# Kernel tuning notes

Hardware: AMD Instinct MI355X
Metric: run time of the kernel (lower is better)

Reference implementation:

```python
import jax, jax.numpy as jnp
import numpy as np

B, C, IMG, P = 64, 3, 224, 16
D, L, H, DH, M, NC = 768, 12, 12, 64, 3072, 1000
INNER = H * DH
PD = C * P * P          # patch_dim = 768
NP = (IMG // P) ** 2    # 196 patches


def setup_inputs() -> dict:
    key = jax.random.key(0)
    ks = jax.random.split(key, 16)
    s = 0.02
    nrm = lambda k, shape: jax.random.normal(k, shape, jnp.float32) * s
    return dict(
        img=jax.random.normal(ks[0], (B, C, IMG, IMG), jnp.float32),
        patch_ln1_g=jnp.ones(PD), patch_ln1_b=jnp.zeros(PD),
        patch_w=nrm(ks[1], (PD, D)), patch_b=jnp.zeros(D),
        patch_ln2_g=jnp.ones(D), patch_ln2_b=jnp.zeros(D),
        pos_emb=nrm(ks[2], (1, NP + 1, D)),
        cls_tok=nrm(ks[3], (1, 1, D)),
        attn_ln_g=jnp.ones((L, D)), attn_ln_b=jnp.zeros((L, D)),
        w_qkv=nrm(ks[4], (L, D, 3 * INNER)),
        w_out=nrm(ks[5], (L, INNER, D)), b_out=jnp.zeros((L, D)),
        ff_ln_g=jnp.ones((L, D)), ff_ln_b=jnp.zeros((L, D)),
        ff_w1=nrm(ks[6], (L, D, M)), ff_b1=jnp.zeros((L, M)),
        ff_w2=nrm(ks[7], (L, M, D)), ff_b2=jnp.zeros((L, D)),
        final_ln_g=jnp.ones(D), final_ln_b=jnp.zeros(D),
        head_w=nrm(ks[8], (D, NC)), head_b=jnp.zeros(NC),
    )


def _ln(x, g, b, eps=1e-5):
    m = x.mean(-1, keepdims=True)
    v = ((x - m) ** 2).mean(-1, keepdims=True)
    return (x - m) / jnp.sqrt(v + eps) * g + b


def reference(img, patch_ln1_g, patch_ln1_b, patch_w, patch_b, patch_ln2_g,
              patch_ln2_b, pos_emb, cls_tok, attn_ln_g, attn_ln_b, w_qkv,
              w_out, b_out, ff_ln_g, ff_ln_b, ff_w1, ff_b1, ff_w2, ff_b2,
              final_ln_g, final_ln_b, head_w, head_b):
    b, c, hh, ww = img.shape
    h, w = hh // P, ww // P
    # Rearrange 'b c (h p1) (w p2) -> b (h w) (p1 p2 c)'
    x = img.reshape(b, c, h, P, w, P).transpose(0, 2, 4, 3, 5, 1).reshape(b, h * w, P * P * c)
    x = _ln(x, patch_ln1_g, patch_ln1_b)
    x = x @ patch_w + patch_b
    x = _ln(x, patch_ln2_g, patch_ln2_b)
    n = x.shape[1]
    x = jnp.concatenate([jnp.broadcast_to(cls_tok, (b, 1, x.shape[-1])), x], axis=1)
    x = x + pos_emb[:, : n + 1]
    scale = DH ** -0.5
    for l in range(L):
        xn = _ln(x, attn_ln_g[l], attn_ln_b[l])
        qkv = xn @ w_qkv[l]  # [b, n+1, 3*inner]
        q, k, v = jnp.split(qkv, 3, axis=-1)
        sp = lambda t: t.reshape(b, -1, H, DH).transpose(0, 2, 1, 3)  # b h n d
        q, k, v = sp(q), sp(k), sp(v)
        # softmax variant: exp(scores*scale), normalize by sum + eps (no max-subtract, faithful to source)
        numer = jnp.exp(jnp.einsum('bhid,bhjd->bhij', q, k) * scale)
        attn = numer / (numer.sum(-1, keepdims=True) + 1e-8)
        out = jnp.einsum('bhij,bhjd->bhid', attn, v)
        out = out.transpose(0, 2, 1, 3).reshape(b, -1, INNER)
        x = out @ w_out[l] + b_out[l] + x
        xn = _ln(x, ff_ln_g[l], ff_ln_b[l])
        hid = jax.nn.gelu(xn @ ff_w1[l] + ff_b1[l], approximate=False)
        x = hid @ ff_w2[l] + ff_b2[l] + x
    x = _ln(x, final_ln_g, final_ln_b)
    return x[:, 0] @ head_w + head_b
```

## Files before the change

### kernel.cpp

```cpp
#include <hip/hip_runtime.h>
#include <hip/hip_bf16.h>
#include <math.h>

#define B_     64
#define NTOK   197
#define NPATCH 196
#define D768   768
#define NL     12
#define NH     12
#define MFF    3072
#define NCLS   1000
#define ROWS   (B_ * NTOK)
#define PROWS  (B_ * NPATCH)
#define ROWS_PAD 12672

typedef unsigned short ushort;
typedef __bf16 bf16x8 __attribute__((ext_vector_type(8)));
typedef float  f32x4  __attribute__((ext_vector_type(4)));
typedef unsigned short u16x4 __attribute__((ext_vector_type(4)));
typedef unsigned short u16x2 __attribute__((ext_vector_type(2)));

__device__ __forceinline__ ushort f2b(float f) {
  __hip_bfloat16 h = __float2bfloat16(f);
  return *reinterpret_cast<ushort*>(&h);
}
__device__ __forceinline__ float b2f(ushort u) {
  unsigned int v = ((unsigned int)u) << 16;
  float f;
  __builtin_memcpy(&f, &v, 4);
  return f;
}

__device__ __forceinline__ void gload16(const ushort* g, ushort* lds) {
  __builtin_amdgcn_global_load_lds((const __attribute__((address_space(1))) void*)g,
                                   (__attribute__((address_space(3))) void*)lds, 16, 0, 0);
}

__device__ __forceinline__ float gelu_f(float v) {
  float t = v * fmaf(0.0713548162726f, v * v, 1.5957691216f);
  return v / (1.0f + __expf(-t));
}

__device__ __forceinline__ void block_mean_rstd(float s, float sq, float& mean, float& rstd) {
#pragma unroll
  for (int off = 32; off; off >>= 1) { s += __shfl_xor(s, off); sq += __shfl_xor(sq, off); }
  __shared__ float ss[4], ssq[4];
  int w = threadIdx.x >> 6;
  if ((threadIdx.x & 63) == 0) { ss[w] = s; ssq[w] = sq; }
  __syncthreads();
  s  = ss[0] + ss[1] + ss[2] + ss[3];
  sq = ssq[0] + ssq[1] + ssq[2] + ssq[3];
  mean = s * (1.0f / 768.0f);
  float var = sq * (1.0f / 768.0f) - mean * mean;
  rstd = rsqrtf(var + 1e-5f);
}

__global__ __launch_bounds__(256) void ln_rows_b(const ushort* __restrict__ in, long in_stride,
                                                 const float* __restrict__ g,
                                                 const float* __restrict__ bta,
                                                 ushort* __restrict__ out) {
  const ushort* xr = in + (size_t)blockIdx.x * in_stride;
  int t = threadIdx.x;
  float v0 = 0.f, v1 = 0.f, v2 = 0.f, v3 = 0.f;
  if (t < 192) {
    u16x4 xv = *(const u16x4*)(xr + t * 4);
    v0 = b2f(xv[0]); v1 = b2f(xv[1]); v2 = b2f(xv[2]); v3 = b2f(xv[3]);
  }
  float mean, rstd;
  block_mean_rstd(v0 + v1 + v2 + v3,
                  v0 * v0 + v1 * v1 + v2 * v2 + v3 * v3, mean, rstd);
  if (t < 192) {
    f32x4 gv = *(const f32x4*)(g + t * 4);
    f32x4 bv = *(const f32x4*)(bta + t * 4);
    u16x4 o = { f2b((v0 - mean) * rstd * gv[0] + bv[0]),
                f2b((v1 - mean) * rstd * gv[1] + bv[1]),
                f2b((v2 - mean) * rstd * gv[2] + bv[2]),
                f2b((v3 - mean) * rstd * gv[3] + bv[3]) };
    *(u16x4*)(out + (size_t)blockIdx.x * 768 + t * 4) = o;
  }
}

__global__ __launch_bounds__(256) void patch_ln1(const float* __restrict__ img,
                                                 const float* __restrict__ g,
                                                 const float* __restrict__ bta,
                                                 ushort* __restrict__ xp) {
  int pidx = blockIdx.x;
  int b = pidx / NPATCH, hw = pidx % NPATCH;
  int ph = hw / 14, pw = hw % 14;
  int t = threadIdx.x;
  float v[3];
#pragma unroll
  for (int u = 0; u < 3; ++u) {
    int k = t + u * 256;
    int c = k % 3, p2 = (k / 3) & 15, p1 = k / 48;
    v[u] = img[(((size_t)b * 3 + c) * 224 + ph * 16 + p1) * 224 + pw * 16 + p2];
  }
  float mean, rstd;
  block_mean_rstd(v[0] + v[1] + v[2], v[0] * v[0] + v[1] * v[1] + v[2] * v[2], mean, rstd);
  ushort* o = xp + (size_t)pidx * 768;
#pragma unroll
  for (int u = 0; u < 3; ++u) { int k = t + u * 256; o[k] = f2b((v[u] - mean) * rstd * g[k] + bta[k]); }
}

__global__ __launch_bounds__(256) void ln2_pos(const float* __restrict__ xe,
                                               const float* __restrict__ g,
                                               const float* __restrict__ bta,
                                               const float* __restrict__ pos,
                                               ushort* __restrict__ x) {
  int pidx = blockIdx.x;
  int b = pidx / NPATCH, i = pidx % NPATCH;
  const float* xr = xe + (size_t)pidx * 768;
  int t = threadIdx.x;
  float v0 = xr[t], v1 = xr[t + 256], v2 = xr[t + 512];
  float mean, rstd;
  block_mean_rstd(v0 + v1 + v2, v0 * v0 + v1 * v1 + v2 * v2, mean, rstd);
  const float* p = pos + (size_t)(1 + i) * 768;
  ushort* o = x + ((size_t)b * NTOK + 1 + i) * 768;
  o[t]       = f2b((v0 - mean) * rstd * g[t]       + bta[t]       + p[t]);
  o[t + 256] = f2b((v1 - mean) * rstd * g[t + 256] + bta[t + 256] + p[t + 256]);
  o[t + 512] = f2b((v2 - mean) * rstd * g[t + 512] + bta[t + 512] + p[t + 512]);
}

__global__ __launch_bounds__(256) void cls_init(const float* __restrict__ cls_tok,
                                                const float* __restrict__ pos,
                                                ushort* __restrict__ x) {
  int b = blockIdx.x, t = threadIdx.x;
  ushort* o = x + (size_t)b * NTOK * 768;
#pragma unroll
  for (int u = 0; u < 3; ++u) { int k = t + u * 256; o[k] = f2b(cls_tok[k] + pos[k]); }
}

__global__ __launch_bounds__(256) void transpose_cast(const float* __restrict__ W,
                                                      ushort* __restrict__ Wt,
                                                      int K, int N) {
  __shared__ float t[32][33];
  int n0 = blockIdx.x * 32, k0 = blockIdx.y * 32;
  int tx = threadIdx.x, ty = threadIdx.y;
#pragma unroll
  for (int u = 0; u < 32; u += 8) {
    int n = n0 + tx;
    t[ty + u][tx] = (n < N) ? W[(size_t)(k0 + ty + u) * N + n] : 0.f;
  }
  __syncthreads();
#pragma unroll
  for (int u = 0; u < 32; u += 8) {
    int n = n0 + ty + u;
    if (n < N) Wt[(size_t)n * K + k0 + tx] = f2b(t[tx][ty + u]);
  }
}

__device__ __forceinline__ void transpose_layer64(int bid,
                                                  const float* wq, const float* wo,
                                                  const float* w1, const float* w2,
                                                  ushort* tq, ushort* to,
                                                  ushort* t1, ushort* t2) {
  const float* W; ushort* Wt; int K, N, xt;
  if (bid < 432)       {             W = wq; Wt = tq; K = 768;  N = 2304; xt = 36; }
  else if (bid < 576)  { bid -= 432; W = wo; Wt = to; K = 768;  N = 768;  xt = 12; }
  else if (bid < 1152) { bid -= 576; W = w1; Wt = t1; K = 768;  N = 3072; xt = 48; }
  else                 { bid -= 1152; W = w2; Wt = t2; K = 3072; N = 768; xt = 12; }
  int n0 = (bid % xt) * 64, k0 = (bid / xt) * 64;
  __shared__ float t[64][65];
  int id = threadIdx.x;
  int tx = id & 15, ty = id >> 4;
#pragma unroll
  for (int u = 0; u < 4; ++u) {
    int k = ty + 16 * u;
    f32x4 v = *(const f32x4*)(W + (size_t)(k0 + k) * N + n0 + tx * 4);
    t[k][tx * 4 + 0] = v[0]; t[k][tx * 4 + 1] = v[1];
    t[k][tx * 4 + 2] = v[2]; t[k][tx * 4 + 3] = v[3];
  }
  __syncthreads();
  int wx = id & 31, wy = id >> 5;
#pragma unroll
  for (int u = 0; u < 8; ++u) {
    int n = wy + 8 * u;
    u16x2 o = { f2b(t[wx * 2][n]), f2b(t[wx * 2 + 1][n]) };
    *(u16x2*)(Wt + (size_t)(n0 + n) * K + k0 + wx * 2) = o;
  }
}

__global__ __launch_bounds__(256) void transpose4(const float* __restrict__ wq,
                                                  const float* __restrict__ wo,
                                                  const float* __restrict__ w1,
                                                  const float* __restrict__ w2,
                                                  ushort* __restrict__ tq,
                                                  ushort* __restrict__ to,
                                                  ushort* __restrict__ t1,
                                                  ushort* __restrict__ t2) {
  transpose_layer64(blockIdx.x, wq, wo, w1, w2, tq, to, t1, t2);
}

__global__ __launch_bounds__(256) void transpose_all(const float* __restrict__ wq,
                                                     const float* __restrict__ wo,
                                                     const float* __restrict__ w1,
                                                     const float* __restrict__ w2,
                                                     ushort* __restrict__ tq,
                                                     ushort* __restrict__ to,
                                                     ushort* __restrict__ t1,
                                                     ushort* __restrict__ t2) {
  int l = blockIdx.x / 1728, bid = blockIdx.x % 1728;
  transpose_layer64(bid,
                    wq + (size_t)l * 768 * 2304, wo + (size_t)l * 768 * 768,
                    w1 + (size_t)l * 768 * MFF,  w2 + (size_t)l * MFF * 768,
                    tq + (size_t)l * 2304 * 768, to + (size_t)l * 768 * 768,
                    t1 + (size_t)l * MFF * 768,  t2 + (size_t)l * 768 * MFF);
}

template<int EP, int RESID, int OBF>
__global__ __launch_bounds__(256, 4) void gemm_v6(const ushort* __restrict__ A,
                                                  const ushort* __restrict__ Bt,
                                                  const float* __restrict__ bias,
                                                  const void* __restrict__ resid,
                                                  void* __restrict__ Cv,
                                                  int M, int N, int K) {
  __shared__ ushort smem[2 * 8192];

  const int tid = threadIdx.x;
  const int w = tid >> 6, l = tid & 63;
  const int fr = l & 15, fc = l >> 4;

  const int ntx = gridDim.x;
  const int nwg = ntx * gridDim.y;
  const int orig = blockIdx.y * ntx + blockIdx.x;
  const int q = nwg >> 3, r = nwg & 7, xcd = orig & 7, idx = orig >> 3;
  const int wg = (xcd < r ? xcd * (q + 1) : r * (q + 1) + (xcd - r) * q) + idx;
  const int row0 = (wg / ntx) * 128, col0 = (wg % ntx) * 128;

  const int wr = (w >> 1) * 64, wc = (w & 1) * 64;

  const int srow = tid >> 2;
  const int sg = (tid & 3) ^ ((srow >> 1) & 3);
  const ushort* pA0 = A  + (size_t)(row0 + srow) * K + sg * 8;
  const ushort* pA1 = A  + (size_t)(row0 + 64 + srow) * K + sg * 8;
  const ushort* pB0 = Bt + (size_t)(col0 + srow) * K + sg * 8;
  const ushort* pB1 = Bt + (size_t)(col0 + 64 + srow) * K + sg * 8;

  auto stage = [&](int t_, ushort* dst) {
    const int k0 = t_ * 32;
    gload16(pA0 + k0, dst + tid * 8);
    gload16(pA1 + k0, dst + (tid + 256) * 8);
    gload16(pB0 + k0, dst + 4096 + tid * 8);
    gload16(pB1 + k0, dst + 4096 + (tid + 256) * 8);
  };

  int idxA[4], idxB[4];
#pragma unroll
  for (int m = 0; m < 4; ++m) {
    int rA = wr + m * 16 + fr;
    idxA[m] = rA * 32 + ((fc ^ ((rA >> 1) & 3)) << 3);
  }
#pragma unroll
  for (int n = 0; n < 4; ++n) {
    int rB = wc + n * 16 + fr;
    idxB[n] = rB * 32 + ((fc ^ ((rB >> 1) & 3)) << 3);
  }

  f32x4 acc[4][4] = {};

  auto compute = [&](const ushort* As) {
    const ushort* Bs = As + 4096;
    bf16x8 a_[4], b_[4];
#pragma unroll
    for (int m = 0; m < 4; ++m) a_[m] = *(const bf16x8*)(As + idxA[m]);
#pragma unroll
    for (int n = 0; n < 4; ++n) b_[n] = *(const bf16x8*)(Bs + idxB[n]);
#pragma unroll
    for (int m = 0; m < 4; ++m)
#pragma unroll
      for (int n = 0; n < 4; ++n)
        acc[m][n] = __builtin_amdgcn_mfma_f32_16x16x32_bf16(b_[n], a_[m], acc[m][n], 0, 0, 0);
  };

#define VM4() asm volatile("s_waitcnt vmcnt(4)" ::: "memory")
#define VM0() asm volatile("s_waitcnt vmcnt(0)" ::: "memory")

  const int NT = K >> 5;

  stage(0, smem);
  for (int t = 0; t < NT; t += 2) {
    if (t + 1 < NT) { stage(t + 1, smem + 8192); VM4(); } else VM0();
    __builtin_amdgcn_s_barrier();
    compute(smem);
    __builtin_amdgcn_s_barrier();
    if (t + 1 < NT) {
      if (t + 2 < NT) { stage(t + 2, smem); VM4(); } else VM0();
      __builtin_amdgcn_s_barrier();
      compute(smem + 8192);
      __builtin_amdgcn_s_barrier();
    }
  }
#undef VM4
#undef VM0

  if (!OBF) {
    float* Cf = (float*)Cv;
#pragma unroll
    for (int m = 0; m < 4; ++m) {
      int row = row0 + wr + m * 16 + fr;
      if (row >= M) continue;
#pragma unroll
      for (int n = 0; n < 4; ++n) {
        int col = col0 + wc + n * 16 + fc * 4;
        f32x4 v = acc[m][n];
        if (bias) v += *(const f32x4*)(bias + col);
        if (EP) {
#pragma unroll
          for (int rr = 0; rr < 4; ++rr) v[rr] = gelu_f(v[rr]);
        }
        if (RESID) v += *(const f32x4*)((const float*)resid + (size_t)row * N + col);
        *(f32x4*)(Cf + (size_t)row * N + col) = v;
      }
    }
  } else {
    __syncthreads();
    ushort* Cw = smem + w * 4096;
#pragma unroll
    for (int m = 0; m < 4; ++m) {
      int rl = m * 16 + fr;
      int row = row0 + wr + rl;
#pragma unroll
      for (int n = 0; n < 4; ++n) {
        int col = col0 + wc + n * 16 + fc * 4;
        f32x4 v = acc[m][n];
        if (bias) v += *(const f32x4*)(bias + col);
        if (EP) {
#pragma unroll
          for (int rr = 0; rr < 4; ++rr) v[rr] = gelu_f(v[rr]);
        }
        if (RESID) {
          u16x4 rv = *(const u16x4*)((const ushort*)resid + (size_t)row * N + col);
#pragma unroll
          for (int rr = 0; rr < 4; ++rr) v[rr] += b2f(rv[rr]);
        }
        u16x4 pk = { f2b(v[0]), f2b(v[1]), f2b(v[2]), f2b(v[3]) };
        int s = (n * 4 + fc) ^ (rl & 7);
        *(u16x4*)(Cw + rl * 64 + s * 4) = pk;
      }
    }
    ushort* Cb = (ushort*)Cv;
#pragma unroll
    for (int pp = 0; pp < 16; ++pp) {
      int rl = pp * 4 + (l >> 4);
      int cs = l & 15;
      u16x4 pk = *(const u16x4*)(Cw + rl * 64 + ((cs ^ (rl & 7)) * 4));
      int row = row0 + wr + rl;
      if (row < M) *(u16x4*)(Cb + (size_t)row * N + col0 + wc + cs * 4) = pk;
    }
  }
}

template<int EP, int RESID, int OBF>
__global__ __launch_bounds__(256, 2) void gemm_v7(const ushort* __restrict__ A,
                                                  const ushort* __restrict__ Bt,
                                                  const float* __restrict__ bias,
                                                  const float* __restrict__ resid,
                                                  void* __restrict__ Cv,
                                                  int M, int N, int K) {
  __shared__ ushort smem[2 * 12288];

  const int tid = threadIdx.x;
  const int w = tid >> 6, l = tid & 63;
  const int fr = l & 15, fc = l >> 4;

  const int ntx = gridDim.x;
  const int nwg = ntx * gridDim.y;
  const int orig = blockIdx.y * ntx + blockIdx.x;
  const int q = nwg >> 3, r = nwg & 7, xcd = orig & 7, idx = orig >> 3;
  const int wg = (xcd < r ? xcd * (q + 1) : r * (q + 1) + (xcd - r) * q) + idx;
  const int row0 = (wg / ntx) * 128, col0 = (wg % ntx) * 256;

  const int wrow = (w >> 1) * 64, wcol = (w & 1) * 128;

  const int srow = tid >> 2;
  const int sg = (tid & 3) ^ ((srow >> 1) & 3);
  const ushort* pA0 = A  + (size_t)(row0 + srow) * K + sg * 8;
  const ushort* pA1 = A  + (size_t)(row0 + 64 + srow) * K + sg * 8;
  const ushort* pB0 = Bt + (size_t)(col0 + srow) * K + sg * 8;
  const ushort* pB1 = Bt + (size_t)(col0 + 64 + srow) * K + sg * 8;
  const ushort* pB2 = Bt + (size_t)(col0 + 128 + srow) * K + sg * 8;
  const ushort* pB3 = Bt + (size_t)(col0 + 192 + srow) * K + sg * 8;

  auto stage = [&](int t_, ushort* dst) {
    const int k0 = t_ * 32;
    gload16(pA0 + k0, dst + tid * 8);
    gload16(pA1 + k0, dst + (tid + 256) * 8);
    ushort* db = dst + 4096;
    gload16(pB0 + k0, db + tid * 8);
    gload16(pB1 + k0, db + (tid + 256) * 8);
    gload16(pB2 + k0, db + (tid + 512) * 8);
    gload16(pB3 + k0, db + (tid + 768) * 8);
  };

  int idxA[4], idxB[8];
#pragma unroll
  for (int m = 0; m < 4; ++m) {
    int rA = wrow + m * 16 + fr;
    idxA[m] = rA * 32 + ((fc ^ ((rA >> 1) & 3)) << 3);
  }
#pragma unroll
  for (int n = 0; n < 8; ++n) {
    int rB = wcol + n * 16 + fr;
    idxB[n] = rB * 32 + ((fc ^ ((rB >> 1) & 3)) << 3);
  }

  f32x4 acc[4][8] = {};

  auto compute = [&](const ushort* As) {
    const ushort* Bs = As + 4096;
    bf16x8 a_[4], b_[8];
#pragma unroll
    for (int m = 0; m < 4; ++m) a_[m] = *(const bf16x8*)(As + idxA[m]);
#pragma unroll
    for (int n = 0; n < 8; ++n) b_[n] = *(const bf16x8*)(Bs + idxB[n]);
#pragma unroll
    for (int m = 0; m < 4; ++m)
#pragma unroll
      for (int n = 0; n < 8; ++n)
        acc[m][n] = __builtin_amdgcn_mfma_f32_16x16x32_bf16(b_[n], a_[m], acc[m][n], 0, 0, 0);
  };

#define VM6() asm volatile("s_waitcnt vmcnt(6)" ::: "memory")
#define VM0() asm volatile("s_waitcnt vmcnt(0)" ::: "memory")

  const int NT = K >> 5;

  stage(0, smem);
  for (int t = 0; t < NT; t += 2) {
    if (t + 1 < NT) { stage(t + 1, smem + 12288); VM6(); } else VM0();
    __builtin_amdgcn_s_barrier();
    compute(smem);
    __builtin_amdgcn_s_barrier();
    if (t + 1 < NT) {
      if (t + 2 < NT) { stage(t + 2, smem); VM6(); } else VM0();
      __builtin_amdgcn_s_barrier();
      compute(smem + 12288);
      __builtin_amdgcn_s_barrier();
    }
  }
#undef VM6
#undef VM0

  if (!OBF) {
    float* Cf = (float*)Cv;
#pragma unroll
    for (int m = 0; m < 4; ++m) {
      int row = row0 + wrow + m * 16 + fr;
      if (row >= M) continue;
#pragma unroll
      for (int n = 0; n < 8; ++n) {
        int col = col0 + wcol + n * 16 + fc * 4;
        f32x4 v = acc[m][n];
        if (bias) v += *(const f32x4*)(bias + col);
        if (EP) {
#pragma unroll
          for (int rr = 0; rr < 4; ++rr) v[rr] = gelu_f(v[rr]);
        }
        if (RESID) v += *(const f32x4*)(resid + (size_t)row * N + col);
        *(f32x4*)(Cf + (size_t)row * N + col) = v;
      }
    }
  } else {
    ushort* Cw = smem + w * 4096;
    ushort* Cb = (ushort*)Cv;
#pragma unroll
    for (int mp = 0; mp < 2; ++mp) {
#pragma unroll
      for (int m2 = 0; m2 < 2; ++m2) {
        int m = mp * 2 + m2;
        int rl = m2 * 16 + fr;
#pragma unroll
        for (int n = 0; n < 8; ++n) {
          int col = col0 + wcol + n * 16 + fc * 4;
          f32x4 v = acc[m][n];
          if (bias) v += *(const f32x4*)(bias + col);
          if (EP) {
#pragma unroll
            for (int rr = 0; rr < 4; ++rr) v[rr] = gelu_f(v[rr]);
          }
          u16x4 pk = { f2b(v[0]), f2b(v[1]), f2b(v[2]), f2b(v[3]) };
          int s = (n * 4 + fc) ^ (rl & 7);
          *(u16x4*)(Cw + rl * 128 + s * 4) = pk;
        }
      }
      asm volatile("s_waitcnt lgkmcnt(0)" ::: "memory");
#pragma unroll
      for (int pp = 0; pp < 16; ++pp) {
        int rl = pp * 2 + (l >> 5);
        int cs = l & 31;
        u16x4 pk = *(const u16x4*)(Cw + rl * 128 + ((cs ^ (rl & 7)) * 4));
        int row = row0 + wrow + mp * 32 + rl;
        if (row < M) *(u16x4*)(Cb + (size_t)row * N + col0 + wcol + cs * 4) = pk;
      }
      asm volatile("s_waitcnt lgkmcnt(0)" ::: "memory");
    }
  }
}

template<int EP, int RESID, int OBF>
__global__ __launch_bounds__(256) void gemm_bt(const ushort* __restrict__ A,
                                               const ushort* __restrict__ Bt,
                                               const float* __restrict__ bias,
                                               const float* __restrict__ resid,
                                               void* __restrict__ C,
                                               int M, int N, int K) {
  __shared__ ushort As[128 * 32];
  __shared__ ushort Bs[128 * 32];
  int tid = threadIdx.x;
  int w = tid >> 6, l = tid & 63;
  int fr = l & 15, fc = l >> 4;
  int row0 = blockIdx.y * 128, col0 = blockIdx.x * 128;
  int wr = (w >> 1) * 64, wc = (w & 1) * 64;

  int srow0 = w * 32 + (l >> 2);
  int srow1 = srow0 + 16;
  int sc0 = (((l & 3) ^ ((srow0 >> 1) & 3)) << 3);
  int sc1 = (((l & 3) ^ ((srow1 >> 1) & 3)) << 3);
  const ushort* ga0 = A  + (size_t)(row0 + srow0) * K + sc0;
  const ushort* ga1 = A  + (size_t)(row0 + srow1) * K + sc1;
  const ushort* gb0 = Bt + (size_t)(col0 + srow0) * K + sc0;
  const ushort* gb1 = Bt + (size_t)(col0 + srow1) * K + sc1;

  int idxA[4], idxB[4];
#pragma unroll
  for (int m = 0; m < 4; ++m) {
    int rA = wr + m * 16 + fr;
    idxA[m] = rA * 32 + ((fc ^ ((rA >> 1) & 3)) << 3);
  }
#pragma unroll
  for (int n = 0; n < 4; ++n) {
    int rB = wc + n * 16 + fr;
    idxB[n] = rB * 32 + ((fc ^ ((rB >> 1) & 3)) << 3);
  }

  f32x4 acc[4][4] = {};

  for (int k0 = 0; k0 < K; k0 += 32) {
    gload16(ga0 + k0, &As[w * 1024]);
    gload16(ga1 + k0, &As[w * 1024 + 512]);
    gload16(gb0 + k0, &Bs[w * 1024]);
    gload16(gb1 + k0, &Bs[w * 1024 + 512]);
    __syncthreads();
    bf16x8 af[4], bfr[4];
#pragma unroll
    for (int m = 0; m < 4; ++m) af[m] = *(const bf16x8*)(As + idxA[m]);
#pragma unroll
    for (int n = 0; n < 4; ++n) bfr[n] = *(const bf16x8*)(Bs + idxB[n]);
#pragma unroll
    for (int m = 0; m < 4; ++m)
#pragma unroll
      for (int n = 0; n < 4; ++n)
        acc[m][n] = __builtin_amdgcn_mfma_f32_16x16x32_bf16(af[m], bfr[n], acc[m][n], 0, 0, 0);
    __syncthreads();
  }

#pragma unroll
  for (int n = 0; n < 4; ++n) {
    int col = col0 + wc + n * 16 + fr;
    if (col >= N) continue;
    float bv = bias ? bias[col] : 0.f;
#pragma unroll
    for (int m = 0; m < 4; ++m) {
#pragma unroll
      for (int rr = 0; rr < 4; ++rr) {
        int row = row0 + wr + m * 16 + fc * 4 + rr;
        if (row >= M) continue;
        float v = acc[m][n][rr] + bv;
        if (EP == 1) v = 0.5f * v * (1.0f + erff(v * 0.70710678118654752f));
        if (RESID) v += resid[(size_t)row * N + col];
        if (OBF) ((ushort*)C)[(size_t)row * N + col] = f2b(v);
        else     ((float*)C)[(size_t)row * N + col]  = v;
      }
    }
  }
}

__global__ __launch_bounds__(256) void attn_mfma(const ushort* __restrict__ qkv,
                                                 ushort* __restrict__ aout) {
  int bid = blockIdx.x;
  int qt = bid & 3;
  int h  = (bid >> 2) % NH;
  int b  = (bid >> 2) / NH;
  int tid = threadIdx.x, w = tid >> 6, l = tid & 63;
  int fr = l & 15, fc = l >> 4;

  __shared__ ushort Vt[64 * 64];
  __shared__ ushort Pl[4 * 16 * 64];

  const size_t brow = (size_t)b * NTOK;
  int q0 = qt * 64 + w * 16;

  bf16x8 qf[2];
  {
    const ushort* qp = qkv + (brow + q0 + fr) * 2304 + h * 64 + fc * 8;
    qf[0] = *(const bf16x8*)qp;
    qf[1] = *(const bf16x8*)(qp + 32);
  }
  float rs[4] = {0.f, 0.f, 0.f, 0.f};
  f32x4 oc[4] = {};

  for (int kt = 0; kt < 4; ++kt) {
    __syncthreads();
    {
      int key = tid >> 2, d0 = (tid & 3) * 16;
      int j = kt * 64 + key;
      bool valid = j < NTOK;
      const ushort* vp = qkv + (brow + j) * 2304 + 1536 + h * 64 + d0;
      ushort vbuf[16];
      if (valid) {
        *(bf16x8*)(vbuf)     = *(const bf16x8*)vp;
        *(bf16x8*)(vbuf + 8) = *(const bf16x8*)(vp + 8);
      } else {
#pragma unroll
        for (int i = 0; i < 16; ++i) vbuf[i] = 0;
      }
#pragma unroll
      for (int i = 0; i < 16; ++i) {
        int d = d0 + i;
        int byte = d * 128 + ((((key >> 3)) ^ (d & 7)) << 4) + (key & 7) * 2;
        Vt[byte >> 1] = vbuf[i];
      }
    }
    f32x4 sc[4];
#pragma unroll
    for (int n = 0; n < 4; ++n) {
      f32x4 z = {};
      const ushort* kp = qkv + (brow + kt * 64 + n * 16 + fr) * 2304 + 768 + h * 64 + fc * 8;
      bf16x8 k0 = *(const bf16x8*)kp;
      bf16x8 k1 = *(const bf16x8*)(kp + 32);
      z = __builtin_amdgcn_mfma_f32_16x16x32_bf16(qf[0], k0, z, 0, 0, 0);
      z = __builtin_amdgcn_mfma_f32_16x16x32_bf16(qf[1], k1, z, 0, 0, 0);
      sc[n] = z;
    }
    float part[4] = {0.f, 0.f, 0.f, 0.f};
#pragma unroll
    for (int n = 0; n < 4; ++n) {
      int j = kt * 64 + n * 16 + fr;
      bool jv = j < NTOK;
#pragma unroll
      for (int rr = 0; rr < 4; ++rr) {
        float e = jv ? __expf(sc[n][rr] * 0.125f) : 0.f;
        part[rr] += e;
        int row = fc * 4 + rr, col = n * 16 + fr;
        int byte = row * 128 + (((col >> 3) ^ (row & 7)) << 4) + (col & 7) * 2;
        Pl[w * 1024 + (byte >> 1)] = f2b(e);
      }
    }
#pragma unroll
    for (int rr = 0; rr < 4; ++rr) {
      float p = part[rr];
      p += __shfl_xor(p, 1); p += __shfl_xor(p, 2);
      p += __shfl_xor(p, 4); p += __shfl_xor(p, 8);
      rs[rr] += p;
    }
    __syncthreads();
#pragma unroll
    for (int ks = 0; ks < 2; ++ks) {
      int prow = fr;
      int pbyte = prow * 128 + (((ks * 4 + fc) ^ (prow & 7)) << 4);
      bf16x8 pf = *(const bf16x8*)(Pl + w * 1024 + (pbyte >> 1));
#pragma unroll
      for (int n = 0; n < 4; ++n) {
        int d = n * 16 + fr;
        int vb = d * 128 + (((ks * 4 + fc) ^ (d & 7)) << 4);
        bf16x8 vf = *(const bf16x8*)(Vt + (vb >> 1));
        oc[n] = __builtin_amdgcn_mfma_f32_16x16x32_bf16(pf, vf, oc[n], 0, 0, 0);
      }
    }
  }
#pragma unroll
  for (int n = 0; n < 4; ++n) {
#pragma unroll
    for (int rr = 0; rr < 4; ++rr) {
      int qq = q0 + fc * 4 + rr;
      if (qq < NTOK) {
        float v = oc[n][rr] / (rs[rr] + 1e-8f);
        aout[(brow + qq) * 768 + h * 64 + n * 16 + fr] = f2b(v);
      }
    }
  }
}

extern "C" void kernel_launch(void* const* d_in, const int* in_sizes, int n_in,
                              void* d_out, int out_size, void* d_ws, size_t ws_size,
                              hipStream_t stream) {
  const float* img       = (const float*)d_in[0];
  const float* p_ln1_g   = (const float*)d_in[1];
  const float* p_ln1_b   = (const float*)d_in[2];
  const float* patch_w   = (const float*)d_in[3];
  const float* patch_b   = (const float*)d_in[4];
  const float* p_ln2_g   = (const float*)d_in[5];
  const float* p_ln2_b   = (const float*)d_in[6];
  const float* pos_emb   = (const float*)d_in[7];
  const float* cls_tok   = (const float*)d_in[8];
  const float* attn_ln_g = (const float*)d_in[9];
  const float* attn_ln_b = (const float*)d_in[10];
  const float* w_qkv     = (const float*)d_in[11];
  const float* w_out     = (const float*)d_in[12];
  const float* b_out     = (const float*)d_in[13];
  const float* ff_ln_g   = (const float*)d_in[14];
  const float* ff_ln_b   = (const float*)d_in[15];
  const float* ff_w1     = (const float*)d_in[16];
  const float* ff_b1     = (const float*)d_in[17];
  const float* ff_w2     = (const float*)d_in[18];
  const float* ff_b2     = (const float*)d_in[19];
  const float* fin_ln_g  = (const float*)d_in[20];
  const float* fin_ln_b  = (const float*)d_in[21];
  const float* head_w    = (const float*)d_in[22];
  const float* head_b    = (const float*)d_in[23];
  float* out = (float*)d_out;

  char* p = (char*)d_ws;
  auto alloc = [&](size_t bytes) { char* r = p; p += (bytes + 255) & ~(size_t)255; return r; };
  ushort* x      = (ushort*)alloc((size_t)ROWS_PAD * 768 * 2);
  ushort* xnb    = (ushort*)alloc((size_t)ROWS_PAD * 768 * 2);
  ushort* qkvb   = (ushort*)alloc((size_t)ROWS_PAD * 2304 * 2);
  ushort* aoutb  = (ushort*)alloc((size_t)ROWS_PAD * 768 * 2);
  ushort* pwt    = (ushort*)alloc((size_t)768 * 768 * 2);
  ushort* hwt    = (ushort*)alloc((size_t)1024 * 768 * 2);
  ushort* xclsb  = (ushort*)alloc((size_t)128 * 768 * 2);
  ushort* hidb   = qkvb;
  ushort* xpb    = xnb;
  float*  xe     = (float*)qkvb;

  const size_t SQ = (size_t)2304 * 768, SO = (size_t)768 * 768, S1 = (size_t)MFF * 768;
  size_t used = (size_t)(p - (char*)d_ws);
  bool oneshot = (used + 12 * (SQ + SO + 2 * S1) * 2 + 4096) <= ws_size;
  int nw = oneshot ? 12 : 1;
  ushort* wtq = (ushort*)alloc(nw * SQ * 2);
  ushort* wto = (ushort*)alloc(nw * SO * 2);
  ushort* wt1 = (ushort*)alloc(nw * S1 * 2);
  ushort* wt2 = (ushort*)alloc(nw * S1 * 2);

  dim3 blk(256), tblk(32, 8);

  transpose_cast<<<dim3(24, 24), tblk, 0, stream>>>(patch_w, pwt, 768, 768);
  transpose_cast<<<dim3(32, 24), tblk, 0, stream>>>(head_w, hwt, 768, 1000);
  if (oneshot)
    transpose_all<<<12 * 1728, blk, 0, stream>>>(w_qkv, w_out, ff_w1, ff_w2,
                                                 wtq, wto, wt1, wt2);
  patch_ln1<<<PROWS, blk, 0, stream>>>(img, p_ln1_g, p_ln1_b, xpb);
  gemm_v6<0, 0, 0><<<dim3(6, 98), blk, 0, stream>>>(xpb, pwt, patch_b, nullptr, xe,
                                                    PROWS, 768, 768);
  ln2_pos<<<PROWS, blk, 0, stream>>>(xe, p_ln2_g, p_ln2_b, pos_emb, x);
  cls_init<<<B_, blk, 0, stream>>>(cls_tok, pos_emb, x);

  for (int l = 0; l < NL; ++l) {
    ushort* tq = wtq + (oneshot ? (size_t)l * SQ : 0);
    ushort* to = wto + (oneshot ? (size_t)l * SO : 0);
    ushort* t1 = wt1 + (oneshot ? (size_t)l * S1 : 0);
    ushort* t2 = wt2 + (oneshot ? (size_t)l * S1 : 0);
    if (!oneshot)
      transpose4<<<1728, blk, 0, stream>>>(w_qkv + (size_t)l * 768 * 2304,
                                           w_out + (size_t)l * 768 * 768,
                                           ff_w1 + (size_t)l * 768 * MFF,
                                           ff_w2 + (size_t)l * MFF * 768,
                                           tq, to, t1, t2);

    ln_rows_b<<<ROWS, blk, 0, stream>>>(x, 768, attn_ln_g + (size_t)l * 768,
                                        attn_ln_b + (size_t)l * 768, xnb);
    gemm_v7<0, 0, 1><<<dim3(9, 99), blk, 0, stream>>>(xnb, tq, nullptr, nullptr, qkvb,
                                                      ROWS, 2304, 768);
    attn_mfma<<<B_ * NH * 4, blk, 0, stream>>>(qkvb, aoutb);
    gemm_v6<0, 1, 1><<<dim3(6, 99), blk, 0, stream>>>(aoutb, to, b_out + (size_t)l * 768,
                                                      x, x, ROWS, 768, 768);
    ln_rows_b<<<ROWS, blk, 0, stream>>>(x, 768, ff_ln_g + (size_t)l * 768,
                                        ff_ln_b + (size_t)l * 768, xnb);
    gemm_v7<1, 0, 1><<<dim3(12, 99), blk, 0, stream>>>(xnb, t1, ff_b1 + (size_t)l * MFF,
                                                       nullptr, hidb, ROWS, MFF, 768);
    gemm_v6<0, 1, 1><<<dim3(6, 99), blk, 0, stream>>>(hidb, t2, ff_b2 + (size_t)l * 768,
                                                      x, x, ROWS, 768, MFF);
  }

  ln_rows_b<<<B_, blk, 0, stream>>>(x, (long)NTOK * 768, fin_ln_g, fin_ln_b, xclsb);
  gemm_bt<0, 0, 0><<<dim3(8, 1), blk, 0, stream>>>(xclsb, hwt, head_b, nullptr, out,
                                                   B_, NCLS, 768);
}
```

Before: 4.234 ms.

## Use 256x256 tiles with 8 waves and triple-buffered LDS in QKV/FF1 GEMMs

Replaces the 128x256, 4-wave GEMM used for the QKV and FF1 projections with a 256x256, 512-thread variant that uses dynamic shared memory. The LDS pipeline goes from double to triple buffering, with one barrier per K step, so loads for step t+2 overlap compute of step t. Row padding is raised to 12800 so the larger tiles stay in bounds. The aim is more reuse per loaded tile and fewer barriers, at the cost of one workgroup per CU, 96KB LDS and fewer blocks in the grid.

```diff
diff --git a/kernel.cpp b/kernel.cpp
--- a/kernel.cpp
+++ b/kernel.cpp
@@ -12,7 +12,7 @@
 #define NCLS   1000
 #define ROWS   (B_ * NTOK)
 #define PROWS  (B_ * NPATCH)
-#define ROWS_PAD 12672
+#define ROWS_PAD 12800
 
 typedef unsigned short ushort;
 typedef __bf16 bf16x8 __attribute__((ext_vector_type(8)));
@@ -351,13 +351,13 @@
 }
 
 template<int EP, int RESID, int OBF>
-__global__ __launch_bounds__(256, 2) void gemm_v7(const ushort* __restrict__ A,
+__global__ __launch_bounds__(512, 1) void gemm_v8(const ushort* __restrict__ A,
                                                   const ushort* __restrict__ Bt,
                                                   const float* __restrict__ bias,
-                                                  const float* __restrict__ resid,
+                                                  const void* __restrict__ resid,
                                                   void* __restrict__ Cv,
                                                   int M, int N, int K) {
-  __shared__ ushort smem[2 * 12288];
+  extern __shared__ ushort smem[];
 
   const int tid = threadIdx.x;
   const int w = tid >> 6, l = tid & 63;
@@ -368,28 +368,23 @@
   const int orig = blockIdx.y * ntx + blockIdx.x;
   const int q = nwg >> 3, r = nwg & 7, xcd = orig & 7, idx = orig >> 3;
   const int wg = (xcd < r ? xcd * (q + 1) : r * (q + 1) + (xcd - r) * q) + idx;
-  const int row0 = (wg / ntx) * 128, col0 = (wg % ntx) * 256;
+  const int row0 = (wg / ntx) * 256, col0 = (wg % ntx) * 256;
 
   const int wrow = (w >> 1) * 64, wcol = (w & 1) * 128;
 
   const int srow = tid >> 2;
   const int sg = (tid & 3) ^ ((srow >> 1) & 3);
   const ushort* pA0 = A  + (size_t)(row0 + srow) * K + sg * 8;
-  const ushort* pA1 = A  + (size_t)(row0 + 64 + srow) * K + sg * 8;
+  const ushort* pA1 = A  + (size_t)(row0 + 128 + srow) * K + sg * 8;
   const ushort* pB0 = Bt + (size_t)(col0 + srow) * K + sg * 8;
-  const ushort* pB1 = Bt + (size_t)(col0 + 64 + srow) * K + sg * 8;
-  const ushort* pB2 = Bt + (size_t)(col0 + 128 + srow) * K + sg * 8;
-  const ushort* pB3 = Bt + (size_t)(col0 + 192 + srow) * K + sg * 8;
+  const ushort* pB1 = Bt + (size_t)(col0 + 128 + srow) * K + sg * 8;
 
   auto stage = [&](int t_, ushort* dst) {
     const int k0 = t_ * 32;
     gload16(pA0 + k0, dst + tid * 8);
-    gload16(pA1 + k0, dst + (tid + 256) * 8);
-    ushort* db = dst + 4096;
-    gload16(pB0 + k0, db + tid * 8);
-    gload16(pB1 + k0, db + (tid + 256) * 8);
-    gload16(pB2 + k0, db + (tid + 512) * 8);
-    gload16(pB3 + k0, db + (tid + 768) * 8);
+    gload16(pA1 + k0, dst + (tid + 512) * 8);
+    gload16(pB0 + k0, dst + 8192 + tid * 8);
+    gload16(pB1 + k0, dst + 8192 + (tid + 512) * 8);
   };
 
   int idxA[4], idxB[8];
@@ -407,7 +402,7 @@
   f32x4 acc[4][8] = {};
 
   auto compute = [&](const ushort* As) {
-    const ushort* Bs = As + 4096;
+    const ushort* Bs = As + 8192;
     bf16x8 a_[4], b_[8];
 #pragma unroll
     for (int m = 0; m < 4; ++m) a_[m] = *(const bf16x8*)(As + idxA[m]);
@@ -420,25 +415,29 @@
         acc[m][n] = __builtin_amdgcn_mfma_f32_16x16x32_bf16(b_[n], a_[m], acc[m][n], 0, 0, 0);
   };
 
-#define VM6() asm volatile("s_waitcnt vmcnt(6)" ::: "memory")
+#define VM4() asm volatile("s_waitcnt vmcnt(4)" ::: "memory")
 #define VM0() asm volatile("s_waitcnt vmcnt(0)" ::: "memory")
 
   const int NT = K >> 5;
 
   stage(0, smem);
-  for (int t = 0; t < NT; t += 2) {
-    if (t + 1 < NT) { stage(t + 1, smem + 12288); VM6(); } else VM0();
-    __builtin_amdgcn_s_barrier();
-    compute(smem);
-    __builtin_amdgcn_s_barrier();
+  stage(1, smem + 16384);
+  VM4();
+  __builtin_amdgcn_s_barrier();
+
+  int bi = 0, si = 2;
+  for (int t = 0; t < NT; ++t) {
+    const bool more2 = (t + 2 < NT);
+    if (more2) stage(t + 2, smem + si * 16384);
+    compute(smem + bi * 16384);
     if (t + 1 < NT) {
-      if (t + 2 < NT) { stage(t + 2, smem); VM6(); } else VM0();
+      if (more2) VM4(); else VM0();
       __builtin_amdgcn_s_barrier();
-      compute(smem + 12288);
-      __builtin_amdgcn_s_barrier();
-    }
-  }
-#undef VM6
+    }
+    bi = (bi == 2) ? 0 : bi + 1;
+    si = (si == 2) ? 0 : si + 1;
+  }
+#undef VM4
 #undef VM0
 
   if (!OBF) {
@@ -456,11 +455,12 @@
 #pragma unroll
           for (int rr = 0; rr < 4; ++rr) v[rr] = gelu_f(v[rr]);
         }
-        if (RESID) v += *(const f32x4*)(resid + (size_t)row * N + col);
+        if (RESID) v += *(const f32x4*)((const float*)resid + (size_t)row * N + col);
         *(f32x4*)(Cf + (size_t)row * N + col) = v;
       }
     }
   } else {
+    __syncthreads();
     ushort* Cw = smem + w * 4096;
     ushort* Cb = (ushort*)Cv;
 #pragma unroll
@@ -710,6 +710,11 @@
   const float* head_b    = (const float*)d_in[23];
   float* out = (float*)d_out;
 
+  (void)hipFuncSetAttribute((const void*)gemm_v8<0, 0, 1>,
+                            hipFuncAttributeMaxDynamicSharedMemorySize, 98304);
+  (void)hipFuncSetAttribute((const void*)gemm_v8<1, 0, 1>,
+                            hipFuncAttributeMaxDynamicSharedMemorySize, 98304);
+
   char* p = (char*)d_ws;
   auto alloc = [&](size_t bytes) { char* r = p; p += (bytes + 255) & ~(size_t)255; return r; };
   ushort* x      = (ushort*)alloc((size_t)ROWS_PAD * 768 * 2);
@@ -732,7 +737,7 @@
   ushort* wt1 = (ushort*)alloc(nw * S1 * 2);
   ushort* wt2 = (ushort*)alloc(nw * S1 * 2);
 
-  dim3 blk(256), tblk(32, 8);
+  dim3 blk(256), blk8(512), tblk(32, 8);
 
   transpose_cast<<<dim3(24, 24), tblk, 0, stream>>>(patch_w, pwt, 768, 768);
   transpose_cast<<<dim3(32, 24), tblk, 0, stream>>>(head_w, hwt, 768, 1000);
@@ -759,15 +764,15 @@
 
     ln_rows_b<<<ROWS, blk, 0, stream>>>(x, 768, attn_ln_g + (size_t)l * 768,
                                         attn_ln_b + (size_t)l * 768, xnb);
-    gemm_v7<0, 0, 1><<<dim3(9, 99), blk, 0, stream>>>(xnb, tq, nullptr, nullptr, qkvb,
-                                                      ROWS, 2304, 768);
+    gemm_v8<0, 0, 1><<<dim3(9, 50), blk8, 98304, stream>>>(xnb, tq, nullptr, nullptr, qkvb,
+                                                           ROWS, 2304, 768);
     attn_mfma<<<B_ * NH * 4, blk, 0, stream>>>(qkvb, aoutb);
     gemm_v6<0, 1, 1><<<dim3(6, 99), blk, 0, stream>>>(aoutb, to, b_out + (size_t)l * 768,
                                                       x, x, ROWS, 768, 768);
     ln_rows_b<<<ROWS, blk, 0, stream>>>(x, 768, ff_ln_g + (size_t)l * 768,
                                         ff_ln_b + (size_t)l * 768, xnb);
-    gemm_v7<1, 0, 1><<<dim3(12, 99), blk, 0, stream>>>(xnb, t1, ff_b1 + (size_t)l * MFF,
-                                                       nullptr, hidb, ROWS, MFF, 768);
+    gemm_v8<1, 0, 1><<<dim3(12, 50), blk8, 98304, stream>>>(xnb, t1, ff_b1 + (size_t)l * MFF,
+                                                            nullptr, hidb, ROWS, MFF, 768);
     gemm_v6<0, 1, 1><<<dim3(6, 99), blk, 0, stream>>>(hidb, t2, ff_b2 + (size_t)l * 768,
                                                       x, x, ROWS, 768, MFF);
   }
```

New measurement: 4.411 ms. +4.2%, slower.
